# Optimization experiments

Hardware: AMD Instinct MI355X
Metric: run time of the kernel (lower is better)

The kernel has to match this reference:

```python
import jax, jax.numpy as jnp
import numpy as np

NUM_INST = 32
EPS = 1e-5
DN = ('NCHW', 'OIHW', 'NCHW')
# torch ConvTranspose2d weight shapes are (in_ch, out_ch, kh, kw) for layers 4,5,6
W_SHAPES = [(32, 3, 7, 7), (64, 32, 3, 3), (128, 64, 3, 3), (256, 128, 3, 3),
            (256, 128, 3, 3), (128, 64, 3, 3), (64, 32, 3, 3), (3, 32, 7, 7)]


def _conv(x, w, b, stride=1, pad=0):
    y = jax.lax.conv_general_dilated(x, w, (stride, stride), ((pad, pad), (pad, pad)),
                                     dimension_numbers=DN)
    return y + b[None, :, None, None]


def _convT(x, w, b):
    # torch ConvTranspose2d(k=3, s=2, p=1): flip kernel, swap in/out axes,
    # lhs_dilation=2, effective pad = k-1-p = 1. Output H -> 2H-1.
    wt = jnp.flip(w, (2, 3)).transpose(1, 0, 2, 3)
    y = jax.lax.conv_general_dilated(x, wt, (1, 1), ((1, 1), (1, 1)),
                                     lhs_dilation=(2, 2), dimension_numbers=DN)
    return y + b[None, :, None, None]


def _inorm(x):
    # InstanceNorm2d(affine=False): normalize each (n, c) plane over HxW
    m = jnp.mean(x, axis=(2, 3), keepdims=True)
    v = jnp.var(x, axis=(2, 3), keepdims=True)
    return (x - m) * jax.lax.rsqrt(v + EPS)


def _rpad(x, p):
    return jnp.pad(x, ((0, 0), (0, 0), (p, p), (p, p)), mode='reflect')


def _net(x, ws, bs):
    x = jax.nn.relu(_inorm(_conv(_rpad(x, 3), ws[0], bs[0])))        # 7x7, 3->32
    for i in (1, 2, 3):                                               # stride-2 down
        x = jax.nn.relu(_inorm(_conv(x, ws[i], bs[i], stride=2, pad=1)))
    for i in (4, 5, 6):                                               # stride-2 up
        x = jax.nn.relu(_inorm(_convT(x, ws[i], bs[i])))
    return jnp.tanh(_conv(_rpad(x, 3), ws[7], bs[7]))                 # 7x7, 32->3


def _segment_mean(outputs, inst):
    # Replace every pixel with the mean of its instance (pooled over the whole
    # batch, per channel) -- fused form of the original double python loop.
    N, C, H, W = outputs.shape
    ids = inst[:, 0].reshape(-1)                                # [N*H*W]
    feats = outputs.transpose(0, 2, 3, 1).reshape(-1, C)        # [N*H*W, C]
    sums = jax.ops.segment_sum(feats, ids, num_segments=NUM_INST)
    cnt = jax.ops.segment_sum(jnp.ones((ids.shape[0],), feats.dtype), ids,
                              num_segments=NUM_INST)
    means = sums / jnp.maximum(cnt, 1.0)[:, None]               # [NUM_INST, C]
    return means[ids].reshape(N, H, W, C).transpose(0, 3, 1, 2)


def setup_inputs() -> dict:
    key = jax.random.key(0)
    ks = jax.random.split(key, 2 + len(W_SHAPES))
    d = {
        'x': jax.random.normal(ks[0], (8, 3, 256, 256), dtype=jnp.float32),
        'inst': jax.random.randint(ks[1], (8, 1, 249, 249), 0, NUM_INST, dtype=jnp.int32),
    }
    for i, s in enumerate(W_SHAPES):
        out_ch = s[1] if i in (4, 5, 6) else s[0]
        d[f'w{i}'] = jax.random.normal(ks[2 + i], s, dtype=jnp.float32) * 0.05
        d[f'b{i}'] = jnp.zeros((out_ch,), dtype=jnp.float32)
    return d


def reference(x, inst, w0, b0, w1, b1, w2, b2, w3, b3, w4, b4, w5, b5, w6, b6, w7, b7):
    ws = (w0, w1, w2, w3, w4, w5, w6, w7)
    bs = (b0, b1, b2, b3, b4, b5, b6, b7)
    out = _net(x, ws, bs)                                       # [8, 3, 249, 249]
    return _segment_mean(out, inst)
```

## Files before the change

kernel.cpp:

```cpp
#include <hip/hip_runtime.h>
#include <math.h>


#define IDIV(a, b) (((a) + (b) - 1) / (b))

__device__ __forceinline__ int reflect_i(int i, int n) {
    i = i < 0 ? -i : i;
    return i >= n ? 2 * n - 2 - i : i;
}

__device__ __forceinline__ float ldb(const char* base, int boff) {
    return *(const float*)(base + boff);
}

template <int OCPT>
__device__ __forceinline__ void stats_block_store(
    const float* sv, const float* ssv, float* __restrict__ spart,
    float* __restrict__ sspart, int P, int tile, int pc0) {
    __shared__ float redS[OCPT], redSS[OCPT];
    if (threadIdx.x < OCPT) { redS[threadIdx.x] = 0.f; redSS[threadIdx.x] = 0.f; }
    __syncthreads();
    int lane = threadIdx.x & 63;
#pragma unroll
    for (int j = 0; j < OCPT; ++j) {
        float s = sv[j], ss = ssv[j];
#pragma unroll
        for (int o = 32; o > 0; o >>= 1) {
            s += __shfl_down(s, o);
            ss += __shfl_down(ss, o);
        }
        if (lane == 0) { atomicAdd(&redS[j], s); atomicAdd(&redSS[j], ss); }
    }
    __syncthreads();
    if (threadIdx.x < OCPT) {
        spart[(size_t)tile * P + pc0 + threadIdx.x] = redS[threadIdx.x];
        sspart[(size_t)tile * P + pc0 + threadIdx.x] = redSS[threadIdx.x];
    }
}

__global__ __launch_bounds__(64) void stat_reduce_mi(
    const float* __restrict__ sp, const float* __restrict__ ssp,
    float* __restrict__ mean, float* __restrict__ inv, int P, int nT,
    float rcp_plane) {
    int p = blockIdx.x;
    float a = 0.f, bsum = 0.f;
    for (int t = threadIdx.x; t < nT; t += 64) {
        a += sp[(size_t)t * P + p];
        bsum += ssp[(size_t)t * P + p];
    }
#pragma unroll
    for (int o = 32; o > 0; o >>= 1) {
        a += __shfl_down(a, o);
        bsum += __shfl_down(bsum, o);
    }
    if (threadIdx.x == 0) {
        float m = a * rcp_plane;
        float var = bsum * rcp_plane - m * m;
        mean[p] = m;
        inv[p] = rsqrtf(var + 1e-5f);
    }
}

template <int CIN, int OCPT>
__global__ __launch_bounds__(256) void conv7_v3s(
    const float* __restrict__ x, const float* __restrict__ w,
    const float* __restrict__ b, float* __restrict__ y,
    float* __restrict__ spart, float* __restrict__ sspart, int P,
    int Cout, int H, int W) {
    int tx = threadIdx.x & 15, ty = threadIdx.x >> 4;
    int tilesX = IDIV(W, 16);
    int ow = (blockIdx.x % tilesX) * 16 + tx;
    int oh = (blockIdx.x / tilesX) * 16 + ty;
    int oc0 = blockIdx.y * OCPT;
    int n = blockIdx.z;

    int offrB[7], iwsB[7];
#pragma unroll
    for (int k = 0; k < 7; ++k) {
        offrB[k] = reflect_i(oh + k - 3, H) * W * 4;
        iwsB[k] = reflect_i(ow + k - 3, W) * 4;
    }

    float acc[OCPT];
#pragma unroll
    for (int j = 0; j < OCPT; ++j) acc[j] = 0.f;

    const char* xb = (const char*)x + (size_t)n * CIN * H * W * 4;
    for (int ic = 0; ic < CIN; ++ic) {
        const char* xp = xb + (size_t)ic * (H * W) * 4;
        float v[49];
#pragma unroll
        for (int kh = 0; kh < 7; ++kh) {
#pragma unroll
            for (int kw = 0; kw < 7; ++kw)
                v[kh * 7 + kw] = ldb(xp, offrB[kh] + iwsB[kw]);
        }
        const float* wp = w + ((size_t)oc0 * CIN + ic) * 49;
#pragma unroll
        for (int j = 0; j < OCPT; ++j) {
#pragma unroll
            for (int t = 0; t < 49; ++t)
                acc[j] += v[t] * wp[(size_t)j * CIN * 49 + t];
        }
    }
    float sv[OCPT], ssv[OCPT];
#pragma unroll
    for (int j = 0; j < OCPT; ++j) {
        float r = acc[j] + b[oc0 + j];
        y[(((size_t)n * Cout + oc0 + j) * H + oh) * W + ow] = r;
        sv[j] = r;
        ssv[j] = r * r;
    }
    stats_block_store<OCPT>(sv, ssv, spart, sspart, P, blockIdx.x, n * Cout + oc0);
}

template <int CINTOT, int ICPB, int OCPT>
__global__ __launch_bounds__(256) void conv7_part(
    const float* __restrict__ x, const float* __restrict__ w,
    float* __restrict__ part, size_t PS, int H, int W) {
    int tx = threadIdx.x & 15, ty = threadIdx.x >> 4;
    int tilesX = IDIV(W, 16);
    int ow = (blockIdx.x % tilesX) * 16 + tx;
    int oh = (blockIdx.x / tilesX) * 16 + ty;
    int ks = blockIdx.y;
    int n = blockIdx.z;
    if (ow >= W || oh >= H) return;

    int offrB[7], iwsB[7];
#pragma unroll
    for (int k = 0; k < 7; ++k) {
        offrB[k] = reflect_i(oh + k - 3, H) * W * 4;
        iwsB[k] = reflect_i(ow + k - 3, W) * 4;
    }

    float acc[OCPT];
#pragma unroll
    for (int j = 0; j < OCPT; ++j) acc[j] = 0.f;

    const char* xb = (const char*)x + (size_t)n * CINTOT * H * W * 4;
    const int ic0 = ks * ICPB;
    for (int icl = 0; icl < ICPB; ++icl) {
        int ic = ic0 + icl;
        const char* xp = xb + (size_t)ic * (H * W) * 4;
        float v[49];
#pragma unroll
        for (int kh = 0; kh < 7; ++kh) {
#pragma unroll
            for (int kw = 0; kw < 7; ++kw)
                v[kh * 7 + kw] = ldb(xp, offrB[kh] + iwsB[kw]);
        }
        const float* wp = w + (size_t)ic * 49;
#pragma unroll
        for (int j = 0; j < OCPT; ++j) {
#pragma unroll
            for (int t = 0; t < 49; ++t)
                acc[j] += v[t] * wp[(size_t)j * CINTOT * 49 + t];
        }
    }
#pragma unroll
    for (int j = 0; j < OCPT; ++j)
        part[(size_t)ks * PS + (((size_t)n * OCPT + j) * H + oh) * W + ow] = acc[j];
}

template <int CIN, int ICB, int OCPT>
__global__ __launch_bounds__(256) void conv3s2_v3s(
    const float* __restrict__ x, const float* __restrict__ w,
    const float* __restrict__ b, float* __restrict__ y,
    float* __restrict__ spart, float* __restrict__ sspart, int P,
    int Cout, int Hin, int Win, int Hout, int Wout) {
    int tx = threadIdx.x & 15, ty = threadIdx.x >> 4;
    int tilesX = Wout >> 4;
    int ow = (blockIdx.x % tilesX) * 16 + tx;
    int oh = (blockIdx.x / tilesX) * 16 + ty;
    int oc0 = blockIdx.y * OCPT;
    int n = blockIdx.z;

    int ih0 = oh * 2 - 1, iw0 = ow * 2 - 1;
    int boff[9];
    float mm[9];
#pragma unroll
    for (int kh = 0; kh < 3; ++kh) {
        int ih = ih0 + kh;
        int ihc = min(max(ih, 0), Hin - 1);
        float mr = (ih >= 0 && ih < Hin) ? 1.f : 0.f;
#pragma unroll
        for (int kw = 0; kw < 3; ++kw) {
            int iw = iw0 + kw;
            int iwc = min(max(iw, 0), Win - 1);
            float mc = (iw >= 0 && iw < Win) ? 1.f : 0.f;
            boff[kh * 3 + kw] = (ihc * Win + iwc) * 4;
            mm[kh * 3 + kw] = mr * mc;
        }
    }

    float acc[OCPT];
#pragma unroll
    for (int j = 0; j < OCPT; ++j) acc[j] = 0.f;

    const char* xb = (const char*)x + (size_t)n * CIN * Hin * Win * 4;
    for (int ic0 = 0; ic0 < CIN; ic0 += ICB) {
        float v[ICB][9];
#pragma unroll
        for (int icl = 0; icl < ICB; ++icl) {
            const char* xp = xb + (size_t)(ic0 + icl) * (Hin * Win) * 4;
#pragma unroll
            for (int t = 0; t < 9; ++t) v[icl][t] = ldb(xp, boff[t]) * mm[t];
        }
#pragma unroll
        for (int icl = 0; icl < ICB; ++icl) {
            const float* wp = w + ((size_t)oc0 * CIN + ic0 + icl) * 9;
#pragma unroll
            for (int j = 0; j < OCPT; ++j) {
#pragma unroll
                for (int t = 0; t < 9; ++t)
                    acc[j] += v[icl][t] * wp[(size_t)j * CIN * 9 + t];
            }
        }
    }
    float sv[OCPT], ssv[OCPT];
#pragma unroll
    for (int j = 0; j < OCPT; ++j) {
        float r = acc[j] + b[oc0 + j];
        y[(((size_t)n * Cout + oc0 + j) * Hout + oh) * Wout + ow] = r;
        sv[j] = r;
        ssv[j] = r * r;
    }
    stats_block_store<OCPT>(sv, ssv, spart, sspart, P, blockIdx.x, n * Cout + oc0);
}

template <int CIN, int ICB, int OCPT>
__global__ __launch_bounds__(256) void convt3_v4s(
    const float* __restrict__ x, const float* __restrict__ w,
    const float* __restrict__ b, float* __restrict__ y,
    float* __restrict__ spart, float* __restrict__ sspart, int P,
    int Cout, int Hin, int Win, int Hout, int Wout) {
    int tx = threadIdx.x & 15, ty = threadIdx.x >> 4;
    int tilesX = IDIV(Win, 16);
    int qx = (blockIdx.x % tilesX) * 16 + tx;
    int qy = (blockIdx.x / tilesX) * 16 + ty;
    int oc0 = blockIdx.y * OCPT;
    int n = blockIdx.z;
    bool valid = (qx < Win) && (qy < Hin);
    int qxc = min(qx, Win - 1), qyc = min(qy, Hin - 1);
    bool xin = valid && (qx + 1 < Win), yin = valid && (qy + 1 < Hin);
    int o01 = xin ? 1 : 0, o10 = yin ? Win : 0;
    float m01 = xin ? 1.f : 0.f, m10 = yin ? 1.f : 0.f, m11 = m01 * m10;

    int p00 = (qyc * Win + qxc) * 4;
    int p01 = p00 + o01 * 4;
    int p10 = p00 + o10 * 4;
    int p11 = p00 + (o01 + o10) * 4;

    float a00[OCPT], a01[OCPT], a10[OCPT], a11[OCPT];
#pragma unroll
    for (int j = 0; j < OCPT; ++j) { a00[j] = a01[j] = a10[j] = a11[j] = 0.f; }

    const char* xb = (const char*)x + (size_t)n * CIN * Hin * Win * 4;
    const int HWb = Hin * Win * 4;

    float va[ICB][4], vb[ICB][4];
    auto load = [&](float (&v)[ICB][4], int ic0) {
#pragma unroll
        for (int icl = 0; icl < ICB; ++icl) {
            const char* xp = xb + (size_t)(ic0 + icl) * HWb;
            v[icl][0] = ldb(xp, p00);
            v[icl][1] = ldb(xp, p01) * m01;
            v[icl][2] = ldb(xp, p10) * m10;
            v[icl][3] = ldb(xp, p11) * m11;
        }
    };
    auto fma = [&](const float (&v)[ICB][4], int ic0) {
#pragma unroll
        for (int icl = 0; icl < ICB; ++icl) {
            const float* wp = w + ((size_t)(ic0 + icl) * Cout + oc0) * 9;
#pragma unroll
            for (int j = 0; j < OCPT; ++j) {
                const float* wj = wp + j * 9;
                float w0 = wj[0], w1 = wj[1], w2 = wj[2];
                float w3 = wj[3], w4 = wj[4], w5 = wj[5];
                float w6 = wj[6], w7 = wj[7], w8 = wj[8];
                a00[j] += w4 * v[icl][0];
                a01[j] += w5 * v[icl][0] + w3 * v[icl][1];
                a10[j] += w7 * v[icl][0] + w1 * v[icl][2];
                a11[j] += w8 * v[icl][0] + w6 * v[icl][1] + w2 * v[icl][2] + w0 * v[icl][3];
            }
        }
    };

    load(va, 0);
    for (int ic0 = 0; ic0 < CIN; ic0 += 2 * ICB) {
        load(vb, ic0 + ICB);
        fma(va, ic0);
        load(va, min(ic0 + 2 * ICB, CIN - ICB));
        fma(vb, ic0 + ICB);
    }

    int oh = 2 * qy, ow = 2 * qx;
    float sv[OCPT], ssv[OCPT];
#pragma unroll
    for (int j = 0; j < OCPT; ++j) {
        float s = 0.f, ss = 0.f;
        if (valid) {
            float bb = b[oc0 + j];
            float* yp = y + (((size_t)n * Cout + oc0 + j) * Hout + oh) * Wout + ow;
            float t00 = a00[j] + bb;
            yp[0] = t00; s += t00; ss += t00 * t00;
            if (xin) { float t = a01[j] + bb; yp[1] = t; s += t; ss += t * t; }
            if (yin) { float t = a10[j] + bb; yp[Wout] = t; s += t; ss += t * t; }
            if (xin && yin) { float t = a11[j] + bb; yp[Wout + 1] = t; s += t; ss += t * t; }
        }
        sv[j] = s; ssv[j] = ss;
    }
    stats_block_store<OCPT>(sv, ssv, spart, sspart, P, blockIdx.x, n * Cout + oc0);
}

__global__ void inorm_apply4(float* __restrict__ x, const float* __restrict__ mean,
                             const float* __restrict__ inv, int plane4) {
    int pc = blockIdx.y;
    int i = blockIdx.x * 256 + threadIdx.x;
    if (i >= plane4) return;
    float m = mean[pc], iv = inv[pc];
    float4* p = (float4*)(x + (size_t)pc * plane4 * 4);
    float4 v = p[i];
    v.x = fmaxf(0.f, (v.x - m) * iv);
    v.y = fmaxf(0.f, (v.y - m) * iv);
    v.z = fmaxf(0.f, (v.z - m) * iv);
    v.w = fmaxf(0.f, (v.w - m) * iv);
    p[i] = v;
}

__global__ void inorm_apply1(float* __restrict__ x, const float* __restrict__ mean,
                             const float* __restrict__ inv, int plane) {
    int pc = blockIdx.y;
    int i = blockIdx.x * 256 + threadIdx.x;
    if (i >= plane) return;
    float m = mean[pc], iv = inv[pc];
    size_t idx = (size_t)pc * plane + i;
    x[idx] = fmaxf(0.f, (x[idx] - m) * iv);
}

__global__ void seg_zero(float* __restrict__ bins) {
    if (threadIdx.x < 128) bins[threadIdx.x] = 0.f;
}

__global__ void seg_accum_f(const float* __restrict__ part, const float* __restrict__ b,
                            const int* __restrict__ inst, float* __restrict__ bins,
                            int HW, size_t PS) {
    __shared__ float ls[128];
    for (int i = threadIdx.x; i < 128; i += 256) ls[i] = 0.f;
    __syncthreads();
    int n = blockIdx.y;
    int i = blockIdx.x * 256 + threadIdx.x;
    if (i < HW) {
        int id = inst[(size_t)n * HW + i];
#pragma unroll
        for (int c = 0; c < 3; ++c) {
            size_t off = ((size_t)(n * 3 + c)) * HW + i;
            float v = part[off] + part[PS + off] + part[2 * PS + off] +
                      part[3 * PS + off] + b[c];
            atomicAdd(&ls[id * 3 + c], tanhf(v));
        }
        atomicAdd(&ls[96 + id], 1.0f);
    }
    __syncthreads();
    for (int i2 = threadIdx.x; i2 < 128; i2 += 256)
        if (ls[i2] != 0.f) atomicAdd(&bins[i2], ls[i2]);
}

__global__ void seg_scatter(const float* __restrict__ bins, const int* __restrict__ inst,
                            float* __restrict__ out, int HW) {
    int n = blockIdx.y;
    int i = blockIdx.x * 256 + threadIdx.x;
    if (i >= HW) return;
    int id = inst[(size_t)n * HW + i];
    float c = fmaxf(bins[96 + id], 1.0f);
    out[((size_t)n * 3 + 0) * HW + i] = bins[id * 3 + 0] / c;
    out[((size_t)n * 3 + 1) * HW + i] = bins[id * 3 + 1] / c;
    out[((size_t)n * 3 + 2) * HW + i] = bins[id * 3 + 2] / c;
}

extern "C" void kernel_launch(void* const* d_in, const int* in_sizes, int n_in,
                              void* d_out, int out_size, void* d_ws, size_t ws_size,
                              hipStream_t stream) {
    const float* x = (const float*)d_in[0];
    const int* inst = (const int*)d_in[1];
    const float* W[8];
    const float* B[8];
    for (int i = 0; i < 8; ++i) {
        W[i] = (const float*)d_in[2 + 2 * i];
        B[i] = (const float*)d_in[3 + 2 * i];
    }
    float* ws = (float*)d_ws;

    const size_t S = 25165824;
    float* a0 = ws;
    float* a1 = ws + 16777216;
    float* a2 = ws;
    float* a3 = ws + 23068672;
    float* a4 = ws;
    float* a5 = ws + 17165824;
    float* a6 = ws;
    float* PART = ws + 16000000;
    float* mean = ws + S;
    float* inv = mean + 2048;
    float* bins = inv + 2048;
    float* spart = bins + 128;
    float* sspart = spart + 65536;

    conv7_v3s<3, 8><<<dim3(256, 4, 8), 256, 0, stream>>>(
        x, W[0], B[0], a0, spart, sspart, 256, 32, 256, 256);
    stat_reduce_mi<<<dim3(256), 64, 0, stream>>>(spart, sspart, mean, inv, 256, 256, 1.f / 65536.f);
    inorm_apply4<<<dim3(IDIV(16384, 256), 256), 256, 0, stream>>>(a0, mean, inv, 16384);

    conv3s2_v3s<32, 4, 8><<<dim3(64, 8, 8), 256, 0, stream>>>(
        a0, W[1], B[1], a1, spart, sspart, 512, 64, 256, 256, 128, 128);
    stat_reduce_mi<<<dim3(512), 64, 0, stream>>>(spart, sspart, mean, inv, 512, 64, 1.f / 16384.f);
    inorm_apply4<<<dim3(IDIV(4096, 256), 512), 256, 0, stream>>>(a1, mean, inv, 4096);

    conv3s2_v3s<64, 4, 8><<<dim3(16, 16, 8), 256, 0, stream>>>(
        a1, W[2], B[2], a2, spart, sspart, 1024, 128, 128, 128, 64, 64);
    stat_reduce_mi<<<dim3(1024), 64, 0, stream>>>(spart, sspart, mean, inv, 1024, 16, 1.f / 4096.f);
    inorm_apply4<<<dim3(IDIV(1024, 256), 1024), 256, 0, stream>>>(a2, mean, inv, 1024);

    conv3s2_v3s<128, 4, 8><<<dim3(4, 32, 8), 256, 0, stream>>>(
        a2, W[3], B[3], a3, spart, sspart, 2048, 256, 64, 64, 32, 32);
    stat_reduce_mi<<<dim3(2048), 64, 0, stream>>>(spart, sspart, mean, inv, 2048, 4, 1.f / 1024.f);
    inorm_apply4<<<dim3(1, 2048), 256, 0, stream>>>(a3, mean, inv, 256);

    convt3_v4s<256, 4, 4><<<dim3(4, 32, 8), 256, 0, stream>>>(
        a3, W[4], B[4], a4, spart, sspart, 1024, 128, 32, 32, 63, 63);
    stat_reduce_mi<<<dim3(1024), 64, 0, stream>>>(spart, sspart, mean, inv, 1024, 4, 1.f / 3969.f);
    inorm_apply1<<<dim3(IDIV(3969, 256), 1024), 256, 0, stream>>>(a4, mean, inv, 3969);

    convt3_v4s<128, 4, 4><<<dim3(16, 16, 8), 256, 0, stream>>>(
        a4, W[5], B[5], a5, spart, sspart, 512, 64, 63, 63, 125, 125);
    stat_reduce_mi<<<dim3(512), 64, 0, stream>>>(spart, sspart, mean, inv, 512, 16, 1.f / 15625.f);
    inorm_apply1<<<dim3(IDIV(15625, 256), 512), 256, 0, stream>>>(a5, mean, inv, 15625);

    convt3_v4s<64, 4, 4><<<dim3(64, 8, 8), 256, 0, stream>>>(
        a5, W[6], B[6], a6, spart, sspart, 256, 32, 125, 125, 249, 249);
    stat_reduce_mi<<<dim3(256), 64, 0, stream>>>(spart, sspart, mean, inv, 256, 64, 1.f / 62001.f);
    inorm_apply1<<<dim3(IDIV(62001, 256), 256), 256, 0, stream>>>(a6, mean, inv, 62001);

    conv7_part<32, 8, 3><<<dim3(256, 4, 8), 256, 0, stream>>>(a6, W[7], PART, 1488024, 249, 249);

    seg_zero<<<1, 128, 0, stream>>>(bins);
    seg_accum_f<<<dim3(IDIV(62001, 256), 8), 256, 0, stream>>>(
        PART, B[7], inst, bins, 62001, 1488024);
    seg_scatter<<<dim3(IDIV(62001, 256), 8), 256, 0, stream>>>(bins, inst, (float*)d_out, 62001);
}
```

Measured before the change: 1.432 ms.

## Register-block 2x2 output pixels per thread in first conv7 and conv3s2 layers

The first 7x7 reflect-padded conv and the first stride-2 3x3 conv now compute a 2x2 patch of outputs per thread. Each thread loads a shared input window once (8x8 or 5x5) and reuses it across the four outputs, and each weight load is also reused four times. To keep register pressure in check, fewer output channels are handled per block (4 instead of 8), and the grid shapes and stats-reduce tile counts are changed to match. The cost is more registers per thread and fewer blocks per channel group, which could lower occupancy.

```diff
diff --git a/kernel.cpp b/kernel.cpp
--- a/kernel.cpp
+++ b/kernel.cpp
@@ -62,54 +62,159 @@
 }
 
 template <int CIN, int OCPT>
-__global__ __launch_bounds__(256) void conv7_v3s(
+__global__ __launch_bounds__(256) void conv7_sp(
     const float* __restrict__ x, const float* __restrict__ w,
     const float* __restrict__ b, float* __restrict__ y,
     float* __restrict__ spart, float* __restrict__ sspart, int P,
     int Cout, int H, int W) {
     int tx = threadIdx.x & 15, ty = threadIdx.x >> 4;
-    int tilesX = IDIV(W, 16);
-    int ow = (blockIdx.x % tilesX) * 16 + tx;
-    int oh = (blockIdx.x / tilesX) * 16 + ty;
+    int tilesX = W / 32;
+    int owb = (blockIdx.x % tilesX) * 32 + tx * 2;
+    int ohb = (blockIdx.x / tilesX) * 32 + ty * 2;
     int oc0 = blockIdx.y * OCPT;
     int n = blockIdx.z;
 
-    int offrB[7], iwsB[7];
-#pragma unroll
-    for (int k = 0; k < 7; ++k) {
-        offrB[k] = reflect_i(oh + k - 3, H) * W * 4;
-        iwsB[k] = reflect_i(ow + k - 3, W) * 4;
-    }
-
-    float acc[OCPT];
-#pragma unroll
-    for (int j = 0; j < OCPT; ++j) acc[j] = 0.f;
+    int rowB[8], colB[8];
+#pragma unroll
+    for (int k = 0; k < 8; ++k) {
+        rowB[k] = reflect_i(ohb + k - 3, H) * W * 4;
+        colB[k] = reflect_i(owb + k - 3, W) * 4;
+    }
+
+    float acc[OCPT][2][2];
+#pragma unroll
+    for (int j = 0; j < OCPT; ++j)
+#pragma unroll
+        for (int py = 0; py < 2; ++py)
+#pragma unroll
+            for (int px = 0; px < 2; ++px) acc[j][py][px] = 0.f;
 
     const char* xb = (const char*)x + (size_t)n * CIN * H * W * 4;
     for (int ic = 0; ic < CIN; ++ic) {
         const char* xp = xb + (size_t)ic * (H * W) * 4;
-        float v[49];
-#pragma unroll
-        for (int kh = 0; kh < 7; ++kh) {
-#pragma unroll
-            for (int kw = 0; kw < 7; ++kw)
-                v[kh * 7 + kw] = ldb(xp, offrB[kh] + iwsB[kw]);
-        }
+        float v[8][8];
+#pragma unroll
+        for (int r = 0; r < 8; ++r)
+#pragma unroll
+            for (int c = 0; c < 8; ++c)
+                v[r][c] = ldb(xp, rowB[r] + colB[c]);
         const float* wp = w + ((size_t)oc0 * CIN + ic) * 49;
 #pragma unroll
         for (int j = 0; j < OCPT; ++j) {
 #pragma unroll
-            for (int t = 0; t < 49; ++t)
-                acc[j] += v[t] * wp[(size_t)j * CIN * 49 + t];
-        }
-    }
+            for (int kh = 0; kh < 7; ++kh) {
+#pragma unroll
+                for (int kw = 0; kw < 7; ++kw) {
+                    float wv = wp[(size_t)j * CIN * 49 + kh * 7 + kw];
+                    acc[j][0][0] += v[kh][kw] * wv;
+                    acc[j][0][1] += v[kh][kw + 1] * wv;
+                    acc[j][1][0] += v[kh + 1][kw] * wv;
+                    acc[j][1][1] += v[kh + 1][kw + 1] * wv;
+                }
+            }
+        }
+    }
+
     float sv[OCPT], ssv[OCPT];
 #pragma unroll
     for (int j = 0; j < OCPT; ++j) {
-        float r = acc[j] + b[oc0 + j];
-        y[(((size_t)n * Cout + oc0 + j) * H + oh) * W + ow] = r;
-        sv[j] = r;
-        ssv[j] = r * r;
+        float bb = b[oc0 + j];
+        float s = 0.f, ss = 0.f;
+#pragma unroll
+        for (int py = 0; py < 2; ++py) {
+#pragma unroll
+            for (int px = 0; px < 2; ++px) {
+                float r = acc[j][py][px] + bb;
+                y[(((size_t)n * Cout + oc0 + j) * H + ohb + py) * W + owb + px] = r;
+                s += r; ss += r * r;
+            }
+        }
+        sv[j] = s; ssv[j] = ss;
+    }
+    stats_block_store<OCPT>(sv, ssv, spart, sspart, P, blockIdx.x, n * Cout + oc0);
+}
+
+template <int CIN, int OCPT>
+__global__ __launch_bounds__(256) void conv3s2_sp(
+    const float* __restrict__ x, const float* __restrict__ w,
+    const float* __restrict__ b, float* __restrict__ y,
+    float* __restrict__ spart, float* __restrict__ sspart, int P,
+    int Cout, int Hin, int Win, int Hout, int Wout) {
+    int tx = threadIdx.x & 15, ty = threadIdx.x >> 4;
+    int tilesX = Wout / 32;
+    int owb = (blockIdx.x % tilesX) * 32 + tx * 2;
+    int ohb = (blockIdx.x / tilesX) * 32 + ty * 2;
+    int oc0 = blockIdx.y * OCPT;
+    int n = blockIdx.z;
+
+    int rB[5], cB[5];
+    float mr[5], mc[5];
+#pragma unroll
+    for (int u = 0; u < 5; ++u) {
+        int ih = 2 * ohb - 1 + u;
+        int ihc = min(max(ih, 0), Hin - 1);
+        rB[u] = ihc * Win * 4;
+        mr[u] = (ih >= 0 && ih < Hin) ? 1.f : 0.f;
+        int iw = 2 * owb - 1 + u;
+        int iwc = min(max(iw, 0), Win - 1);
+        cB[u] = iwc * 4;
+        mc[u] = (iw >= 0 && iw < Win) ? 1.f : 0.f;
+    }
+    float mm[5][5];
+#pragma unroll
+    for (int u = 0; u < 5; ++u)
+#pragma unroll
+        for (int t = 0; t < 5; ++t) mm[u][t] = mr[u] * mc[t];
+
+    float acc[OCPT][2][2];
+#pragma unroll
+    for (int j = 0; j < OCPT; ++j)
+#pragma unroll
+        for (int py = 0; py < 2; ++py)
+#pragma unroll
+            for (int px = 0; px < 2; ++px) acc[j][py][px] = 0.f;
+
+    const char* xb = (const char*)x + (size_t)n * CIN * Hin * Win * 4;
+    for (int ic = 0; ic < CIN; ++ic) {
+        const char* xp = xb + (size_t)ic * (Hin * Win) * 4;
+        float v[5][5];
+#pragma unroll
+        for (int u = 0; u < 5; ++u)
+#pragma unroll
+            for (int t = 0; t < 5; ++t)
+                v[u][t] = ldb(xp, rB[u] + cB[t]) * mm[u][t];
+        const float* wp = w + ((size_t)oc0 * CIN + ic) * 9;
+#pragma unroll
+        for (int j = 0; j < OCPT; ++j) {
+#pragma unroll
+            for (int kh = 0; kh < 3; ++kh) {
+#pragma unroll
+                for (int kw = 0; kw < 3; ++kw) {
+                    float wv = wp[(size_t)j * CIN * 9 + kh * 3 + kw];
+                    acc[j][0][0] += v[kh][kw] * wv;
+                    acc[j][0][1] += v[kh][kw + 2] * wv;
+                    acc[j][1][0] += v[kh + 2][kw] * wv;
+                    acc[j][1][1] += v[kh + 2][kw + 2] * wv;
+                }
+            }
+        }
+    }
+
+    float sv[OCPT], ssv[OCPT];
+#pragma unroll
+    for (int j = 0; j < OCPT; ++j) {
+        float bb = b[oc0 + j];
+        float s = 0.f, ss = 0.f;
+#pragma unroll
+        for (int py = 0; py < 2; ++py) {
+#pragma unroll
+            for (int px = 0; px < 2; ++px) {
+                float r = acc[j][py][px] + bb;
+                y[(((size_t)n * Cout + oc0 + j) * Hout + ohb + py) * Wout + owb + px] = r;
+                s += r; ss += r * r;
+            }
+        }
+        sv[j] = s; ssv[j] = ss;
     }
     stats_block_store<OCPT>(sv, ssv, spart, sspart, P, blockIdx.x, n * Cout + oc0);
 }
@@ -407,14 +512,14 @@
     float* spart = bins + 128;
     float* sspart = spart + 65536;
 
-    conv7_v3s<3, 8><<<dim3(256, 4, 8), 256, 0, stream>>>(
+    conv7_sp<3, 4><<<dim3(64, 8, 8), 256, 0, stream>>>(
         x, W[0], B[0], a0, spart, sspart, 256, 32, 256, 256);
-    stat_reduce_mi<<<dim3(256), 64, 0, stream>>>(spart, sspart, mean, inv, 256, 256, 1.f / 65536.f);
+    stat_reduce_mi<<<dim3(256), 64, 0, stream>>>(spart, sspart, mean, inv, 256, 64, 1.f / 65536.f);
     inorm_apply4<<<dim3(IDIV(16384, 256), 256), 256, 0, stream>>>(a0, mean, inv, 16384);
 
-    conv3s2_v3s<32, 4, 8><<<dim3(64, 8, 8), 256, 0, stream>>>(
+    conv3s2_sp<32, 4><<<dim3(16, 16, 8), 256, 0, stream>>>(
         a0, W[1], B[1], a1, spart, sspart, 512, 64, 256, 256, 128, 128);
-    stat_reduce_mi<<<dim3(512), 64, 0, stream>>>(spart, sspart, mean, inv, 512, 64, 1.f / 16384.f);
+    stat_reduce_mi<<<dim3(512), 64, 0, stream>>>(spart, sspart, mean, inv, 512, 16, 1.f / 16384.f);
     inorm_apply4<<<dim3(IDIV(4096, 256), 512), 256, 0, stream>>>(a1, mean, inv, 4096);
 
     conv3s2_v3s<64, 4, 8><<<dim3(16, 16, 8), 256, 0, stream>>>(
```

Result: slower. 1.657 ms (+15.8%).

## Stage stride-2 conv input tiles in LDS with float4 cooperative loads

Applied to the files above, without the earlier changes.

Replaces the per-thread direct global loads in the three stride-2 3x3 downsampling convolutions with a cooperative load of a 33x36 input tile per channel group into shared memory, using float4 reads and zero-filling at borders. Each thread then reads its 3x3 windows from LDS, so overlapping input pixels are no longer fetched separately by neighbouring threads. This adds two barriers per channel group, about 19KB of LDS per block, and integer div/mod work in the load loop, which may lower occupancy.

```diff
diff --git a/kernel.cpp b/kernel.cpp
--- a/kernel.cpp
+++ b/kernel.cpp
@@ -163,60 +163,74 @@
 }
 
 template <int CIN, int ICB, int OCPT>
-__global__ __launch_bounds__(256) void conv3s2_v3s(
+__global__ __launch_bounds__(256) void conv3s2_lds(
     const float* __restrict__ x, const float* __restrict__ w,
     const float* __restrict__ b, float* __restrict__ y,
     float* __restrict__ spart, float* __restrict__ sspart, int P,
     int Cout, int Hin, int Win, int Hout, int Wout) {
+    constexpr int RR = 33, CC = 36;
+    __shared__ float s[ICB][RR][CC];
     int tx = threadIdx.x & 15, ty = threadIdx.x >> 4;
     int tilesX = Wout >> 4;
-    int ow = (blockIdx.x % tilesX) * 16 + tx;
-    int oh = (blockIdx.x / tilesX) * 16 + ty;
+    int bx = blockIdx.x % tilesX, by = blockIdx.x / tilesX;
     int oc0 = blockIdx.y * OCPT;
     int n = blockIdx.z;
-
-    int ih0 = oh * 2 - 1, iw0 = ow * 2 - 1;
-    int boff[9];
-    float mm[9];
-#pragma unroll
-    for (int kh = 0; kh < 3; ++kh) {
-        int ih = ih0 + kh;
-        int ihc = min(max(ih, 0), Hin - 1);
-        float mr = (ih >= 0 && ih < Hin) ? 1.f : 0.f;
-#pragma unroll
-        for (int kw = 0; kw < 3; ++kw) {
-            int iw = iw0 + kw;
-            int iwc = min(max(iw, 0), Win - 1);
-            float mc = (iw >= 0 && iw < Win) ? 1.f : 0.f;
-            boff[kh * 3 + kw] = (ihc * Win + iwc) * 4;
-            mm[kh * 3 + kw] = mr * mc;
-        }
-    }
+    int oh = by * 16 + ty, ow = bx * 16 + tx;
+    int ih0 = by * 32 - 1;
+    int c0a = bx * 32 - 4;
+    const int HW = Hin * Win;
 
     float acc[OCPT];
 #pragma unroll
     for (int j = 0; j < OCPT; ++j) acc[j] = 0.f;
 
-    const char* xb = (const char*)x + (size_t)n * CIN * Hin * Win * 4;
+    const float* xn = x + (size_t)n * CIN * HW;
+
     for (int ic0 = 0; ic0 < CIN; ic0 += ICB) {
-        float v[ICB][9];
+        __syncthreads();
+        for (int q = threadIdx.x; q < ICB * RR * 9; q += 256) {
+            int icq = q / (RR * 9), rem = q % (RR * 9);
+            int r = rem / 9, f = rem % 9;
+            int ih = ih0 + r;
+            bool rok = (ih >= 0) && (ih < Hin);
+            int cb = c0a + f * 4;
+            float4 v4;
+            if (rok && cb >= 0) {
+                v4 = *(const float4*)(xn + (size_t)(ic0 + icq) * HW +
+                                      (size_t)ih * Win + cb);
+            } else {
+                float t0 = 0.f, t1 = 0.f, t2 = 0.f, t3 = 0.f;
+                if (rok) {
+                    const float* row = xn + (size_t)(ic0 + icq) * HW + (size_t)ih * Win;
+                    if (cb + 0 >= 0 && cb + 0 < Win) t0 = row[cb + 0];
+                    if (cb + 1 >= 0 && cb + 1 < Win) t1 = row[cb + 1];
+                    if (cb + 2 >= 0 && cb + 2 < Win) t2 = row[cb + 2];
+                    if (cb + 3 >= 0 && cb + 3 < Win) t3 = row[cb + 3];
+                }
+                v4 = make_float4(t0, t1, t2, t3);
+            }
+            *(float4*)&s[icq][r][f * 4] = v4;
+        }
+        __syncthreads();
 #pragma unroll
         for (int icl = 0; icl < ICB; ++icl) {
-            const char* xp = xb + (size_t)(ic0 + icl) * (Hin * Win) * 4;
-#pragma unroll
-            for (int t = 0; t < 9; ++t) v[icl][t] = ldb(xp, boff[t]) * mm[t];
-        }
-#pragma unroll
-        for (int icl = 0; icl < ICB; ++icl) {
+            float v[9];
+#pragma unroll
+            for (int kh = 0; kh < 3; ++kh) {
+#pragma unroll
+                for (int kw = 0; kw < 3; ++kw)
+                    v[kh * 3 + kw] = s[icl][2 * ty + kh][2 * tx + 3 + kw];
+            }
             const float* wp = w + ((size_t)oc0 * CIN + ic0 + icl) * 9;
 #pragma unroll
             for (int j = 0; j < OCPT; ++j) {
 #pragma unroll
                 for (int t = 0; t < 9; ++t)
-                    acc[j] += v[icl][t] * wp[(size_t)j * CIN * 9 + t];
+                    acc[j] += v[t] * wp[(size_t)j * CIN * 9 + t];
             }
         }
     }
+
     float sv[OCPT], ssv[OCPT];
 #pragma unroll
     for (int j = 0; j < OCPT; ++j) {
@@ -412,17 +426,17 @@
     stat_reduce_mi<<<dim3(256), 64, 0, stream>>>(spart, sspart, mean, inv, 256, 256, 1.f / 65536.f);
     inorm_apply4<<<dim3(IDIV(16384, 256), 256), 256, 0, stream>>>(a0, mean, inv, 16384);
 
-    conv3s2_v3s<32, 4, 8><<<dim3(64, 8, 8), 256, 0, stream>>>(
+    conv3s2_lds<32, 4, 8><<<dim3(64, 8, 8), 256, 0, stream>>>(
         a0, W[1], B[1], a1, spart, sspart, 512, 64, 256, 256, 128, 128);
     stat_reduce_mi<<<dim3(512), 64, 0, stream>>>(spart, sspart, mean, inv, 512, 64, 1.f / 16384.f);
     inorm_apply4<<<dim3(IDIV(4096, 256), 512), 256, 0, stream>>>(a1, mean, inv, 4096);
 
-    conv3s2_v3s<64, 4, 8><<<dim3(16, 16, 8), 256, 0, stream>>>(
+    conv3s2_lds<64, 4, 8><<<dim3(16, 16, 8), 256, 0, stream>>>(
         a1, W[2], B[2], a2, spart, sspart, 1024, 128, 128, 128, 64, 64);
     stat_reduce_mi<<<dim3(1024), 64, 0, stream>>>(spart, sspart, mean, inv, 1024, 16, 1.f / 4096.f);
     inorm_apply4<<<dim3(IDIV(1024, 256), 1024), 256, 0, stream>>>(a2, mean, inv, 1024);
 
-    conv3s2_v3s<128, 4, 8><<<dim3(4, 32, 8), 256, 0, stream>>>(
+    conv3s2_lds<128, 4, 8><<<dim3(4, 32, 8), 256, 0, stream>>>(
         a2, W[3], B[3], a3, spart, sspart, 2048, 256, 64, 64, 32, 32);
     stat_reduce_mi<<<dim3(2048), 64, 0, stream>>>(spart, sspart, mean, inv, 2048, 4, 1.f / 1024.f);
     inorm_apply4<<<dim3(1, 2048), 256, 0, stream>>>(a3, mean, inv, 256);
```

Measured after the change: 1.505 ms. 5.1% more time.
